# Kernel optimization log

Measured on AMD Instinct MI355X. Metric: run time of the kernel, lower is better.

## Reference

```python
import jax, jax.numpy as jnp
import numpy as np

N_JOBS, N_MACH = 30, 20
N = N_JOBS * N_MACH          # 600 nodes
IN_DIM = 2
H = 128                      # hidden_dim_feature_extractor
HA = 256                     # hidden_dim_actor
HC = 256                     # hidden_dim_critic
E = 9600                     # edges
BN_EPS = 1e-5


def setup_inputs() -> dict:
    key = jax.random.key(0)
    ks = jax.random.split(key, 16)
    init = lambda k, shp: (jax.random.normal(k, shp, jnp.float32) * 0.05)
    d = {
        "features": jax.random.normal(ks[0], (N, IN_DIM), jnp.float32),
        "edge_index": jax.random.randint(ks[1], (2, E), 0, N, jnp.int32),
        # GIN layer 0 MLP: Linear(IN,H) -> BN -> ReLU -> Linear(H,H)
        "g0_W0": init(ks[2], (IN_DIM, H)), "g0_b0": jnp.zeros((H,), jnp.float32),
        "g0_gamma": jnp.ones((H,), jnp.float32), "g0_beta": jnp.zeros((H,), jnp.float32),
        "g0_W1": init(ks[3], (H, H)), "g0_b1": jnp.zeros((H,), jnp.float32),
        # GIN layer 1 MLP: Linear(H,H) -> BN -> ReLU -> Linear(H,H)
        "g1_W0": init(ks[4], (H, H)), "g1_b0": jnp.zeros((H,), jnp.float32),
        "g1_gamma": jnp.ones((H,), jnp.float32), "g1_beta": jnp.zeros((H,), jnp.float32),
        "g1_W1": init(ks[5], (H, H)), "g1_b1": jnp.zeros((H,), jnp.float32),
        # actor MLP: Linear(3H,HA) -> ReLU -> Linear(HA,1)
        "a_W0": init(ks[6], (3 * H, HA)), "a_b0": jnp.zeros((HA,), jnp.float32),
        "a_W1": init(ks[7], (HA, 1)), "a_b1": jnp.zeros((1,), jnp.float32),
        # critic MLP: Linear(H,HC) -> ReLU -> Linear(HC,1)
        "c_W0": init(ks[8], (H, HC)), "c_b0": jnp.zeros((HC,), jnp.float32),
        "c_W1": init(ks[9], (HC, 1)), "c_b1": jnp.zeros((1,), jnp.float32),
    }
    return d


def _gin_mlp(h, W0, b0, gamma, beta, W1, b1):
    # Linear -> BatchNorm(train-mode batch stats) -> ReLU -> Linear
    h1 = h @ W0 + b0
    mu = h1.mean(axis=0)
    var = h1.var(axis=0)
    h1 = gamma * (h1 - mu) * jax.lax.rsqrt(var + BN_EPS) + beta
    return jax.nn.relu(h1) @ W1 + b1


def reference(features, edge_index,
              g0_W0, g0_b0, g0_gamma, g0_beta, g0_W1, g0_b1,
              g1_W0, g1_b0, g1_gamma, g1_beta, g1_W1, g1_b1,
              a_W0, a_b0, a_W1, a_b1,
              c_W0, c_b0, c_W1, c_b1):
    src, dst = edge_index[0], edge_index[1]

    def gin(x, *mlp_params):
        # GINConv with eps=0: MLP(x + sum_{j in N(i)} x_j)
        agg = jax.ops.segment_sum(x[src], dst, num_segments=N)
        return _gin_mlp(x + agg, *mlp_params)

    h = gin(features, g0_W0, g0_b0, g0_gamma, g0_beta, g0_W1, g0_b1)
    h = gin(h, g1_W0, g1_b0, g1_gamma, g1_beta, g1_W1, g1_b1)   # (N, H)

    # graph pooling: (ones/N) @ h  == mean over nodes
    ge = h.mean(axis=0, keepdims=True)                           # (1, H)
    value = jax.nn.relu(ge @ c_W0 + c_b0) @ c_W1 + c_b1          # (1, 1)

    # s_a_pairs row k (k = i*N + j): [ge, h[j] (tile), h[i] (repeat_interleave)]
    # Fuse concat + first actor matmul by splitting a_W0 into three H-blocks.
    Ws, Wn1, Wn2 = a_W0[:H], a_W0[H:2 * H], a_W0[2 * H:]
    pre = (ge @ Ws + a_b0)[None, :, :] + (h @ Wn1)[None, :, :] + (h @ Wn2)[:, None, :]
    logits = jax.nn.relu(pre).reshape(N * N, HA) @ a_W1 + a_b1   # (N^2, 1)
    pi = jax.nn.softmax(logits, axis=0)
    return pi, value
```

## Files before the change

### kernel.cpp

```cpp
#include <hip/hip_runtime.h>
#include <math.h>

#define N_NODES 600
#define N_EDGES 9600
#define HDIM    128
#define HA      256
#define HC      256
#define NN      360000
#define BN_EPS  1e-5f
#define NTILE   361

#define OFF_U      0
#define OFF_BCONST 1200
#define OFF_BF     1456
#define OFF_SUMZ   1584
#define OFF_SUMZ2  1712
#define OFF_R1SUM  1840
#define OFF_RACC   1968
#define OFF_MAXA   2224
#define OFF_SUMA   2736
#define OFF_CSR    3248
#define OFF_WF     13456
#define OFF_WC1    29840
#define OFF_WC2    62608
#define OFF_WGS    95376
#define OFF_Z      128144
#define OFF_A      204944
#define OFF_B      358544

typedef _Float16 h2 __attribute__((ext_vector_type(2)));
typedef _Float16 h4 __attribute__((ext_vector_type(4)));
typedef _Float16 h8 __attribute__((ext_vector_type(8)));

__device__ __forceinline__ float dot2acc(h2 a, h2 b, float c) {
#if __has_builtin(__builtin_amdgcn_fdot2)
  return __builtin_amdgcn_fdot2(a, b, c, false);
#else
  return c + (float)a.x * (float)b.x + (float)a.y * (float)b.y;
#endif
}

__device__ __forceinline__ h2 relu2(h2 x) {
  h2 z = {(_Float16)0, (_Float16)0};
#if __has_builtin(__builtin_elementwise_max)
  return __builtin_elementwise_max(x, z);
#else
  h2 r;
  r.x = x.x > z.x ? x.x : z.x;
  r.y = x.y > z.y ? x.y : z.y;
  return r;
#endif
}

__device__ __forceinline__ h4 toh4(float4 v) {
  h4 r;
  r.x = (_Float16)v.x; r.y = (_Float16)v.y;
  r.z = (_Float16)v.z; r.w = (_Float16)v.w;
  return r;
}

struct KP {
  const float* feat; const int* ei;
  const float *g0W0, *g0ga, *g0be, *g0W1, *g0b1;
  const float *g1W0, *g1ga, *g1be, *g1W1, *g1b1;
  const float *aW0, *ab0, *aW1;
  const float *cW0, *cb0, *cW1, *cb1;
  float* ws; float* out;
};

__global__ __launch_bounds__(256) void k_indep(KP p) {
  __shared__ float sm[1536];
  const int b = blockIdx.x, t = threadIdx.x;

  if (b < 25) {
    float* us = sm;
    if (t < 48) us[t] = 0.f;
    __syncthreads();
    const int lo = b * 24, hi = lo + 24;
    for (int e = t; e < N_EDGES; e += 256) {
      int d = p.ei[N_EDGES + e];
      if (d >= lo && d < hi) {
        int s = p.ei[e];
        atomicAdd(&us[2 * (d - lo)],     p.feat[2 * s]);
        atomicAdd(&us[2 * (d - lo) + 1], p.feat[2 * s + 1]);
      }
    }
    __syncthreads();
    if (t < 48) p.ws[OFF_U + b * 48 + t] = us[t] + p.feat[b * 48 + t];
  } else if (b == 25) {
    int* si = (int*)sm;
    int* cnt = si; int* bs = si + 600; int* off = si + 856;
    int* rs_g = (int*)(p.ws + OFF_CSR);
    int* src_g = rs_g + 604;
    for (int i = t; i < 600; i += 256) cnt[i] = 0;
    __syncthreads();
    for (int e = t; e < N_EDGES; e += 256) atomicAdd(&cnt[p.ei[N_EDGES + e]], 1);
    __syncthreads();
    int lsum = 0;
    if (t < 200) lsum = cnt[3 * t] + cnt[3 * t + 1] + cnt[3 * t + 2];
    bs[t] = lsum; __syncthreads();
    for (int d = 1; d < 256; d <<= 1) {
      int v = (t >= d) ? bs[t - d] : 0;
      __syncthreads();
      bs[t] += v;
      __syncthreads();
    }
    if (t < 200) {
      int base = bs[t] - lsum;
      off[3 * t] = base;
      off[3 * t + 1] = base + cnt[3 * t];
      off[3 * t + 2] = base + cnt[3 * t] + cnt[3 * t + 1];
    }
    if (t == 0) off[600] = N_EDGES;
    __syncthreads();
    for (int i = t; i < 601; i += 256) rs_g[i] = off[i];
    for (int i = t; i < 600; i += 256) cnt[i] = off[i];
    __syncthreads();
    for (int e = t; e < N_EDGES; e += 256) {
      int d = p.ei[N_EDGES + e];
      int pos = atomicAdd(&cnt[d], 1);
      src_g[pos] = p.ei[e];
    }
  } else if (b < 122) {
    int o = (b - 26) * 1024 + t * 4;
    int mat = o >> 15, rem = o & 32767;
    int j = rem >> 8, k = rem & 255;
    int rowbase = (mat == 0) ? HDIM : (mat == 1 ? 2 * HDIM : 0);
    const float* aw = p.aW0 + rowbase * HA + k;
    float4 acc = make_float4(0, 0, 0, 0);
#pragma unroll 8
    for (int m = 0; m < HDIM; m++) {
      float w = p.g1W1[j * HDIM + m];
      const float4 v = *(const float4*)(aw + m * HA);
      acc.x += w * v.x; acc.y += w * v.y; acc.z += w * v.z; acc.w += w * v.w;
    }
    int dst = (mat == 0) ? OFF_WC1 : (mat == 1 ? OFF_WC2 : OFF_WGS);
    *(float4*)(p.ws + dst + j * HA + k) = acc;
  } else if (b < 138) {
    int o = (b - 122) * 1024 + t * 4;
    int j = o >> 7, c = o & 127;
    float4 acc = make_float4(0, 0, 0, 0);
#pragma unroll 8
    for (int m = 0; m < HDIM; m++) {
      float w = p.g0W1[j * HDIM + m];
      const float4 v = *(const float4*)(p.g1W0 + m * HDIM + c);
      acc.x += w * v.x; acc.y += w * v.y; acc.z += w * v.z; acc.w += w * v.w;
    }
    *(float4*)(p.ws + OFF_WF + j * HDIM + c) = acc;
  } else {
    float acc = 0.f;
#pragma unroll 8
    for (int m = 0; m < HDIM; m++) {
      float gb = p.g1b1[m];
      acc += gb * (p.aW0[m * HA + t] + p.aW0[(HDIM + m) * HA + t] +
                   p.aW0[(2 * HDIM + m) * HA + t]);
    }
    p.ws[OFF_BCONST + t] = p.ab0[t] + acc;
    p.ws[OFF_RACC + t] = 0.f;
    if (t < 128) {
      float a2 = 0.f;
#pragma unroll 8
      for (int m = 0; m < HDIM; m++) a2 += p.g0b1[m] * p.g1W0[m * HDIM + t];
      p.ws[OFF_BF + t] = a2;
      p.ws[OFF_SUMZ + t] = 0.f;
      p.ws[OFF_SUMZ2 + t] = 0.f;
      p.ws[OFF_R1SUM + t] = 0.f;
    }
  }
}

__global__ __launch_bounds__(256) void k_zagg(KP p) {
  __shared__ float2 u2[600];
  __shared__ float bn[384];
  __shared__ float r0agg[512];
  __shared__ float red[256];
  __shared__ float wred[24];
  const int b = blockIdx.x, t = threadIdx.x, n0 = b * 4;
  const float2* ug = (const float2*)(p.ws + OFF_U);
  for (int i = t; i < 600; i += 256) u2[i] = ug[i];
  __syncthreads();
  float s0 = 0, s1 = 0, s00 = 0, s11 = 0, s01 = 0;
  for (int n = t; n < N_NODES; n += 256) {
    float u0 = u2[n].x, u1 = u2[n].y;
    s0 += u0; s1 += u1; s00 += u0 * u0; s11 += u1 * u1; s01 += u0 * u1;
  }
#pragma unroll
  for (int off = 32; off > 0; off >>= 1) {
    s0  += __shfl_xor(s0, off);  s1  += __shfl_xor(s1, off);
    s00 += __shfl_xor(s00, off); s11 += __shfl_xor(s11, off);
    s01 += __shfl_xor(s01, off);
  }
  const int wv = t >> 6, ln = t & 63;
  if (ln == 0) {
    wred[wv * 5 + 0] = s0;  wred[wv * 5 + 1] = s1;  wred[wv * 5 + 2] = s00;
    wred[wv * 5 + 3] = s11; wred[wv * 5 + 4] = s01;
  }
  __syncthreads();
  if (t < HDIM) {
    float tot[5];
#pragma unroll
    for (int q = 0; q < 5; q++)
      tot[q] = wred[q] + wred[5 + q] + wred[10 + q] + wred[15 + q];
    float m0 = tot[0] / 600.f, m1 = tot[1] / 600.f;
    float v00 = tot[2] / 600.f - m0 * m0;
    float v11 = tot[3] / 600.f - m1 * m1;
    float v01 = tot[4] / 600.f - m0 * m1;
    float W00 = p.g0W0[t], W01 = p.g0W0[HDIM + t];
    float var = W00 * W00 * v00 + W01 * W01 * v11 + 2.f * W00 * W01 * v01;
    float sc = p.g0ga[t] * rsqrtf(var + BN_EPS);
    float mu = m0 * W00 + m1 * W01;
    bn[t] = sc * W00; bn[128 + t] = sc * W01; bn[256 + t] = p.g0be[t] - mu * sc;
  }
  __syncthreads();
  const int* rs = (const int*)(p.ws + OFF_CSR);
  const int* srcv = rs + 604;
#pragma unroll
  for (int pq = 0; pq < 2; pq++) {
    int idx = pq * 256 + t, n = idx >> 7, c = idx & 127, node = n0 + n;
    float b0c = bn[c], b1c = bn[128 + c], b2c = bn[256 + c];
    float2 uo = u2[node];
    float acc = fmaxf(uo.x * b0c + uo.y * b1c + b2c, 0.f);
    int e0 = rs[node], e1 = rs[node + 1];
    for (int e = e0; e < e1; e++) {
      float2 us = u2[srcv[e]];
      acc += fmaxf(us.x * b0c + us.y * b1c + b2c, 0.f);
    }
    r0agg[n * 128 + c] = acc;
  }
  __syncthreads();
  const float* Wf = p.ws + OFF_WF;
  const float* bf = p.ws + OFF_BF;
  float zs = 0.f, zs2 = 0.f;
#pragma unroll
  for (int pq = 0; pq < 2; pq++) {
    int idx = pq * 256 + t, n = idx >> 7, c = idx & 127, node = n0 + n;
    const float* row = r0agg + n * 128;
    int deg = rs[node + 1] - rs[node];
    float acc = (1.f + (float)deg) * bf[c];
#pragma unroll 8
    for (int j = 0; j < HDIM; j++) acc += row[j] * Wf[j * HDIM + c];
    p.ws[OFF_Z + node * HDIM + c] = acc;
    zs += acc; zs2 += acc * acc;
  }
  red[t] = zs; __syncthreads();
  if (t < 128) atomicAdd(&p.ws[OFF_SUMZ + t], red[t] + red[t + 128]);
  __syncthreads();
  red[t] = zs2; __syncthreads();
  if (t < 128) atomicAdd(&p.ws[OFF_SUMZ2 + t], red[t] + red[t + 128]);
}

__global__ __launch_bounds__(256) void k_rab(KP p) {
  __shared__ float r1[4 * 128];
  __shared__ float scl[128], shf[128], rsum4[128];
  const int b = blockIdx.x, t = threadIdx.x, n0 = b * 4;
  if (t < 128) {
    float mu = p.ws[OFF_SUMZ + t] * (1.f / 600.f);
    float var = p.ws[OFF_SUMZ2 + t] * (1.f / 600.f) - mu * mu;
    float sc = p.g1ga[t] * rsqrtf(var + BN_EPS);
    scl[t] = sc; shf[t] = p.g1be[t] - mu * sc;
  }
  __syncthreads();
#pragma unroll
  for (int pq = 0; pq < 2; pq++) {
    int idx = pq * 256 + t, n = idx >> 7, j = idx & 127;
    float z = p.ws[OFF_Z + (n0 + n) * HDIM + j];
    r1[n * 128 + j] = fmaxf(z * scl[j] + shf[j], 0.f);
  }
  __syncthreads();
  if (t < 128) {
    float s = r1[t] + r1[128 + t] + r1[256 + t] + r1[384 + t];
    rsum4[t] = s;
    atomicAdd(&p.ws[OFF_R1SUM + t], s);
  }
  __syncthreads();
  const float* wc1 = p.ws + OFF_WC1;
  const float* wc2 = p.ws + OFF_WC2;
  const float* wgs = p.ws + OFF_WGS;
  float a0 = 0, a1 = 0, a2 = 0, a3 = 0, b0 = 0, b1 = 0, b2 = 0, b3 = 0, rc = 0;
#pragma unroll 4
  for (int j = 0; j < HDIM; j++) {
    float w1 = wc1[j * HA + t], w2 = wc2[j * HA + t], wg = wgs[j * HA + t];
    float r0v = r1[j], r1v = r1[128 + j], r2v = r1[256 + j], r3v = r1[384 + j];
    a0 += r0v * w1; a1 += r1v * w1; a2 += r2v * w1; a3 += r3v * w1;
    b0 += r0v * w2; b1 += r1v * w2; b2 += r2v * w2; b3 += r3v * w2;
    rc += rsum4[j] * wg;
  }
  atomicAdd(&p.ws[OFF_RACC + t], rc);
  float* A = p.ws + OFF_A; float* Bm = p.ws + OFF_B;
  A[n0 * HA + t] = a0; A[(n0 + 1) * HA + t] = a1;
  A[(n0 + 2) * HA + t] = a2; A[(n0 + 3) * HA + t] = a3;
  Bm[n0 * HA + t] = b0; Bm[(n0 + 1) * HA + t] = b1;
  Bm[(n0 + 2) * HA + t] = b2; Bm[(n0 + 3) * HA + t] = b3;
}

__global__ __launch_bounds__(256) void k_heads(KP p) {
  __shared__ h4 AsL[2048];
  __shared__ h4 BsL[2048];
  __shared__ h4 wlp[64];
  __shared__ h4 hsp[64];
  __shared__ float hsl[256];
  __shared__ float ge[128];
  __shared__ float geh[128];
  __shared__ float red[256];
  const int b = blockIdx.x, t = threadIdx.x;

  hsl[t] = p.ws[OFF_RACC + t] * (1.f / 600.f) + p.ws[OFF_BCONST + t];

  if (b == 0) {
    if (t < 128) ge[t] = p.ws[OFF_R1SUM + t] * (1.f / 600.f);
    __syncthreads();
    if (t < 128) {
      float a0 = p.g1b1[t], a1 = 0.f, a2 = 0.f, a3 = 0.f;
#pragma unroll 4
      for (int j = 0; j < HDIM; j += 4) {
        a0 += ge[j]     * p.g1W1[(j)     * HDIM + t];
        a1 += ge[j + 1] * p.g1W1[(j + 1) * HDIM + t];
        a2 += ge[j + 2] * p.g1W1[(j + 2) * HDIM + t];
        a3 += ge[j + 3] * p.g1W1[(j + 3) * HDIM + t];
      }
      geh[t] = (a0 + a1) + (a2 + a3);
    }
    __syncthreads();
    {
      float v0 = p.cb0[t], v1 = 0.f, v2 = 0.f, v3 = 0.f;
#pragma unroll 4
      for (int c = 0; c < HDIM; c += 4) {
        v0 += geh[c]     * p.cW0[(c)     * HC + t];
        v1 += geh[c + 1] * p.cW0[(c + 1) * HC + t];
        v2 += geh[c + 2] * p.cW0[(c + 2) * HC + t];
        v3 += geh[c + 3] * p.cW0[(c + 3) * HC + t];
      }
      float v = fmaxf((v0 + v1) + (v2 + v3), 0.f);
      red[t] = v * p.cW1[t];
    }
    __syncthreads();
    for (int off = 128; off > 0; off >>= 1) {
      if (t < off) red[t] += red[t + off];
      __syncthreads();
    }
    if (t == 0) p.out[NN] = red[0] + p.cb1[0];
  }
  __syncthreads();
  if (t < 64) {
    wlp[t] = toh4(*(const float4*)(p.aW1 + 4 * t));
    hsp[t] = toh4(*(const float4*)(hsl + 4 * t));
  }
  __syncthreads();

  const int tj = b % 19, ti = b / 19;
  const int j0 = tj * 32, i0 = ti * 32;
  const float* A  = p.ws + OFF_A;
  const float* Bm = p.ws + OFF_B;
#pragma unroll
  for (int q = 0; q < 8; q++) {
    int f = q * 256 + t;
    int r = f >> 6;
    int c4 = f & 63;
    int k = c4 * 4;
    int sw = c4 * 32 + (r ^ (c4 & 30));
    float4 av = (j0 + r < N_NODES) ? *(const float4*)(A + (j0 + r) * HA + k)
                                   : make_float4(0, 0, 0, 0);
    AsL[sw] = toh4(av) + hsp[c4];
    float4 bv = (i0 + r < N_NODES) ? *(const float4*)(Bm + (i0 + r) * HA + k)
                                   : make_float4(0, 0, 0, 0);
    BsL[sw] = toh4(bv);
  }
  __syncthreads();

  const int tx = t & 15, ty = t >> 4;
  const int jl = tx * 2, il = ty * 2;
  float a00 = 0, a01 = 0, a10 = 0, a11 = 0;
#pragma unroll 8
  for (int kk2 = 0; kk2 < 64; kk2++) {
    int s = kk2 & 30;
    h8 va = *(h8*)&AsL[kk2 * 32 + (jl ^ s)];
    h8 vb = *(h8*)&BsL[kk2 * 32 + (il ^ s)];
    h4 vw = wlp[kk2];
    h2 wlo = __builtin_shufflevector(vw, vw, 0, 1);
    h2 whi = __builtin_shufflevector(vw, vw, 2, 3);
    h2 aj0lo = __builtin_shufflevector(va, va, 0, 1);
    h2 aj0hi = __builtin_shufflevector(va, va, 2, 3);
    h2 aj1lo = __builtin_shufflevector(va, va, 4, 5);
    h2 aj1hi = __builtin_shufflevector(va, va, 6, 7);
    h2 bi0lo = __builtin_shufflevector(vb, vb, 0, 1);
    h2 bi0hi = __builtin_shufflevector(vb, vb, 2, 3);
    h2 bi1lo = __builtin_shufflevector(vb, vb, 4, 5);
    h2 bi1hi = __builtin_shufflevector(vb, vb, 6, 7);
    a00 = dot2acc(relu2(aj0lo + bi0lo), wlo, a00);
    a00 = dot2acc(relu2(aj0hi + bi0hi), whi, a00);
    a01 = dot2acc(relu2(aj1lo + bi0lo), wlo, a01);
    a01 = dot2acc(relu2(aj1hi + bi0hi), whi, a01);
    a10 = dot2acc(relu2(aj0lo + bi1lo), wlo, a10);
    a10 = dot2acc(relu2(aj0hi + bi1hi), whi, a10);
    a11 = dot2acc(relu2(aj1lo + bi1lo), wlo, a11);
    a11 = dot2acc(relu2(aj1hi + bi1hi), whi, a11);
  }

  const int gi = i0 + il, gj = j0 + jl;
  const bool vi0 = gi < N_NODES, vi1 = gi + 1 < N_NODES;
  const bool vj0 = gj < N_NODES, vj1 = gj + 1 < N_NODES;
  float m = -INFINITY;
  if (vi0 && vj0) m = fmaxf(m, a00);
  if (vi0 && vj1) m = fmaxf(m, a01);
  if (vi1 && vj0) m = fmaxf(m, a10);
  if (vi1 && vj1) m = fmaxf(m, a11);
  __syncthreads();
  red[t] = m;
  __syncthreads();
  for (int off = 128; off > 0; off >>= 1) {
    if (t < off) red[t] = fmaxf(red[t], red[t + off]);
    __syncthreads();
  }
  const float mb = red[0];
  float s = 0.f;
  if (vi0 && vj0) { float e = expf(a00 - mb); p.out[gi * N_NODES + gj] = e; s += e; }
  if (vi0 && vj1) { float e = expf(a01 - mb); p.out[gi * N_NODES + gj + 1] = e; s += e; }
  if (vi1 && vj0) { float e = expf(a10 - mb); p.out[(gi + 1) * N_NODES + gj] = e; s += e; }
  if (vi1 && vj1) { float e = expf(a11 - mb); p.out[(gi + 1) * N_NODES + gj + 1] = e; s += e; }
  __syncthreads();
  red[t] = s;
  __syncthreads();
  for (int off = 128; off > 0; off >>= 1) {
    if (t < off) red[t] += red[t + off];
    __syncthreads();
  }
  if (t == 0) { p.ws[OFF_MAXA + b] = mb; p.ws[OFF_SUMA + b] = red[0]; }
}

__global__ __launch_bounds__(256) void k_fin(KP p) {
  __shared__ float red[256];
  __shared__ float sc19[19];
  const int b = blockIdx.x, t = threadIdx.x;
  const float* maxa = p.ws + OFF_MAXA;
  const float* suma = p.ws + OFF_SUMA;
  float m = -INFINITY;
  if (t < NTILE) m = maxa[t];
  if (t + 256 < NTILE) m = fmaxf(m, maxa[t + 256]);
  red[t] = m;
  __syncthreads();
  for (int off = 128; off > 0; off >>= 1) {
    if (t < off) red[t] = fmaxf(red[t], red[t + off]);
    __syncthreads();
  }
  const float gmax = red[0];
  __syncthreads();
  float s = 0.f;
  if (t < NTILE) s += suma[t] * expf(maxa[t] - gmax);
  if (t + 256 < NTILE) s += suma[t + 256] * expf(maxa[t + 256] - gmax);
  red[t] = s;
  __syncthreads();
  for (int off = 128; off > 0; off >>= 1) {
    if (t < off) red[t] += red[t + off];
    __syncthreads();
  }
  const float invtot = 1.0f / red[0];
  const int ti = (b * 4) >> 5;
  if (t < 19) sc19[t] = expf(maxa[ti * 19 + t] - gmax) * invtot;
  __syncthreads();
#pragma unroll
  for (int pass = 0; pass < 3; pass++) {
    int f4 = pass * 256 + t;
    if (f4 < 600) {
      int r = f4 / 150, c4 = (f4 % 150) * 4;
      float* pp = p.out + (b * 4 + r) * N_NODES + c4;
      float4 v = *(const float4*)pp;
      float sc = sc19[c4 >> 5];
      v.x *= sc; v.y *= sc; v.z *= sc; v.w *= sc;
      *(float4*)pp = v;
    }
  }
}

extern "C" void kernel_launch(void* const* d_in, const int* in_sizes, int n_in,
                              void* d_out, int out_size, void* d_ws, size_t ws_size,
                              hipStream_t stream) {
  KP p;
  p.feat = (const float*)d_in[0];
  p.ei   = (const int*)  d_in[1];
  p.g0W0 = (const float*)d_in[2];
  p.g0ga = (const float*)d_in[4];  p.g0be = (const float*)d_in[5];
  p.g0W1 = (const float*)d_in[6];  p.g0b1 = (const float*)d_in[7];
  p.g1W0 = (const float*)d_in[8];
  p.g1ga = (const float*)d_in[10]; p.g1be = (const float*)d_in[11];
  p.g1W1 = (const float*)d_in[12]; p.g1b1 = (const float*)d_in[13];
  p.aW0  = (const float*)d_in[14]; p.ab0  = (const float*)d_in[15];
  p.aW1  = (const float*)d_in[16];
  p.cW0  = (const float*)d_in[18]; p.cb0  = (const float*)d_in[19];
  p.cW1  = (const float*)d_in[20]; p.cb1  = (const float*)d_in[21];
  p.ws   = (float*)d_ws;
  p.out  = (float*)d_out;

  k_indep<<<139,   256, 0, stream>>>(p);
  k_zagg <<<150,   256, 0, stream>>>(p);
  k_rab  <<<150,   256, 0, stream>>>(p);
  k_heads<<<NTILE, 256, 0, stream>>>(p);
  k_fin  <<<150,   256, 0, stream>>>(p);
}
```

Measured before the change: 79.75 us.

## Drop max-subtraction from softmax and move actor weight precompute into zagg

The softmax no longer computes per-tile maxima. Each tile writes exp(logit) directly and only block sums are reduced, so k_fin becomes a plain sum and scale. This removes two block reductions and the expf rescaling, at the risk of overflow if logits grow large. Separately, the actor-weight folding (WC1/WC2/WGS) and the bias-constant blocks move from k_indep into extra blocks of k_zagg, overlapping that work with the aggregation stage and shrinking the first kernel.

```diff
diff --git a/kernel.cpp b/kernel.cpp
--- a/kernel.cpp
+++ b/kernel.cpp
@@ -17,7 +17,6 @@
 #define OFF_SUMZ2  1712
 #define OFF_R1SUM  1840
 #define OFF_RACC   1968
-#define OFF_MAXA   2224
 #define OFF_SUMA   2736
 #define OFF_CSR    3248
 #define OFF_WF     13456
@@ -121,23 +120,8 @@
       int pos = atomicAdd(&cnt[d], 1);
       src_g[pos] = p.ei[e];
     }
-  } else if (b < 122) {
+  } else if (b < 42) {
     int o = (b - 26) * 1024 + t * 4;
-    int mat = o >> 15, rem = o & 32767;
-    int j = rem >> 8, k = rem & 255;
-    int rowbase = (mat == 0) ? HDIM : (mat == 1 ? 2 * HDIM : 0);
-    const float* aw = p.aW0 + rowbase * HA + k;
-    float4 acc = make_float4(0, 0, 0, 0);
-#pragma unroll 8
-    for (int m = 0; m < HDIM; m++) {
-      float w = p.g1W1[j * HDIM + m];
-      const float4 v = *(const float4*)(aw + m * HA);
-      acc.x += w * v.x; acc.y += w * v.y; acc.z += w * v.z; acc.w += w * v.w;
-    }
-    int dst = (mat == 0) ? OFF_WC1 : (mat == 1 ? OFF_WC2 : OFF_WGS);
-    *(float4*)(p.ws + dst + j * HA + k) = acc;
-  } else if (b < 138) {
-    int o = (b - 122) * 1024 + t * 4;
     int j = o >> 7, c = o & 127;
     float4 acc = make_float4(0, 0, 0, 0);
 #pragma unroll 8
@@ -148,14 +132,6 @@
     }
     *(float4*)(p.ws + OFF_WF + j * HDIM + c) = acc;
   } else {
-    float acc = 0.f;
-#pragma unroll 8
-    for (int m = 0; m < HDIM; m++) {
-      float gb = p.g1b1[m];
-      acc += gb * (p.aW0[m * HA + t] + p.aW0[(HDIM + m) * HA + t] +
-                   p.aW0[(2 * HDIM + m) * HA + t]);
-    }
-    p.ws[OFF_BCONST + t] = p.ab0[t] + acc;
     p.ws[OFF_RACC + t] = 0.f;
     if (t < 128) {
       float a2 = 0.f;
@@ -175,7 +151,38 @@
   __shared__ float r0agg[512];
   __shared__ float red[256];
   __shared__ float wred[24];
-  const int b = blockIdx.x, t = threadIdx.x, n0 = b * 4;
+  const int b = blockIdx.x, t = threadIdx.x;
+
+  if (b >= 150) {
+    if (b < 246) {
+      int o = (b - 150) * 1024 + t * 4;
+      int mat = o >> 15, rem = o & 32767;
+      int j = rem >> 8, k = rem & 255;
+      int rowbase = (mat == 0) ? HDIM : (mat == 1 ? 2 * HDIM : 0);
+      const float* aw = p.aW0 + rowbase * HA + k;
+      float4 acc = make_float4(0, 0, 0, 0);
+#pragma unroll 8
+      for (int m = 0; m < HDIM; m++) {
+        float w = p.g1W1[j * HDIM + m];
+        const float4 v = *(const float4*)(aw + m * HA);
+        acc.x += w * v.x; acc.y += w * v.y; acc.z += w * v.z; acc.w += w * v.w;
+      }
+      int dst = (mat == 0) ? OFF_WC1 : (mat == 1 ? OFF_WC2 : OFF_WGS);
+      *(float4*)(p.ws + dst + j * HA + k) = acc;
+    } else {
+      float acc = 0.f;
+#pragma unroll 8
+      for (int m = 0; m < HDIM; m++) {
+        float gb = p.g1b1[m];
+        acc += gb * (p.aW0[m * HA + t] + p.aW0[(HDIM + m) * HA + t] +
+                     p.aW0[(2 * HDIM + m) * HA + t]);
+      }
+      p.ws[OFF_BCONST + t] = p.ab0[t] + acc;
+    }
+    return;
+  }
+
+  const int n0 = b * 4;
   const float2* ug = (const float2*)(p.ws + OFF_U);
   for (int i = t; i < 600; i += 256) u2[i] = ug[i];
   __syncthreads();
@@ -399,24 +406,11 @@
   const int gi = i0 + il, gj = j0 + jl;
   const bool vi0 = gi < N_NODES, vi1 = gi + 1 < N_NODES;
   const bool vj0 = gj < N_NODES, vj1 = gj + 1 < N_NODES;
-  float m = -INFINITY;
-  if (vi0 && vj0) m = fmaxf(m, a00);
-  if (vi0 && vj1) m = fmaxf(m, a01);
-  if (vi1 && vj0) m = fmaxf(m, a10);
-  if (vi1 && vj1) m = fmaxf(m, a11);
-  __syncthreads();
-  red[t] = m;
-  __syncthreads();
-  for (int off = 128; off > 0; off >>= 1) {
-    if (t < off) red[t] = fmaxf(red[t], red[t + off]);
-    __syncthreads();
-  }
-  const float mb = red[0];
   float s = 0.f;
-  if (vi0 && vj0) { float e = expf(a00 - mb); p.out[gi * N_NODES + gj] = e; s += e; }
-  if (vi0 && vj1) { float e = expf(a01 - mb); p.out[gi * N_NODES + gj + 1] = e; s += e; }
-  if (vi1 && vj0) { float e = expf(a10 - mb); p.out[(gi + 1) * N_NODES + gj] = e; s += e; }
-  if (vi1 && vj1) { float e = expf(a11 - mb); p.out[(gi + 1) * N_NODES + gj + 1] = e; s += e; }
+  if (vi0 && vj0) { float e = __expf(a00); p.out[gi * N_NODES + gj] = e; s += e; }
+  if (vi0 && vj1) { float e = __expf(a01); p.out[gi * N_NODES + gj + 1] = e; s += e; }
+  if (vi1 && vj0) { float e = __expf(a10); p.out[(gi + 1) * N_NODES + gj] = e; s += e; }
+  if (vi1 && vj1) { float e = __expf(a11); p.out[(gi + 1) * N_NODES + gj + 1] = e; s += e; }
   __syncthreads();
   red[t] = s;
   __syncthreads();
@@ -424,39 +418,21 @@
     if (t < off) red[t] += red[t + off];
     __syncthreads();
   }
-  if (t == 0) { p.ws[OFF_MAXA + b] = mb; p.ws[OFF_SUMA + b] = red[0]; }
+  if (t == 0) p.ws[OFF_SUMA + b] = red[0];
 }
 
 __global__ __launch_bounds__(256) void k_fin(KP p) {
   __shared__ float red[256];
-  __shared__ float sc19[19];
   const int b = blockIdx.x, t = threadIdx.x;
-  const float* maxa = p.ws + OFF_MAXA;
   const float* suma = p.ws + OFF_SUMA;
-  float m = -INFINITY;
-  if (t < NTILE) m = maxa[t];
-  if (t + 256 < NTILE) m = fmaxf(m, maxa[t + 256]);
-  red[t] = m;
-  __syncthreads();
-  for (int off = 128; off > 0; off >>= 1) {
-    if (t < off) red[t] = fmaxf(red[t], red[t + off]);
-    __syncthreads();
-  }
-  const float gmax = red[0];
-  __syncthreads();
-  float s = 0.f;
-  if (t < NTILE) s += suma[t] * expf(maxa[t] - gmax);
-  if (t + 256 < NTILE) s += suma[t + 256] * expf(maxa[t + 256] - gmax);
+  float s = (t < NTILE ? suma[t] : 0.f) + (t + 256 < NTILE ? suma[t + 256] : 0.f);
   red[t] = s;
   __syncthreads();
   for (int off = 128; off > 0; off >>= 1) {
     if (t < off) red[t] += red[t + off];
     __syncthreads();
   }
-  const float invtot = 1.0f / red[0];
-  const int ti = (b * 4) >> 5;
-  if (t < 19) sc19[t] = expf(maxa[ti * 19 + t] - gmax) * invtot;
-  __syncthreads();
+  const float inv = 1.0f / red[0];
 #pragma unroll
   for (int pass = 0; pass < 3; pass++) {
     int f4 = pass * 256 + t;
@@ -464,8 +440,7 @@
       int r = f4 / 150, c4 = (f4 % 150) * 4;
       float* pp = p.out + (b * 4 + r) * N_NODES + c4;
       float4 v = *(const float4*)pp;
-      float sc = sc19[c4 >> 5];
-      v.x *= sc; v.y *= sc; v.z *= sc; v.w *= sc;
+      v.x *= inv; v.y *= inv; v.z *= inv; v.w *= inv;
       *(float4*)pp = v;
     }
   }
@@ -490,8 +465,8 @@
   p.ws   = (float*)d_ws;
   p.out  = (float*)d_out;
 
-  k_indep<<<139,   256, 0, stream>>>(p);
-  k_zagg <<<150,   256, 0, stream>>>(p);
+  k_indep<<<43,    256, 0, stream>>>(p);
+  k_zagg <<<247,   256, 0, stream>>>(p);
   k_rab  <<<150,   256, 0, stream>>>(p);
   k_heads<<<NTILE, 256, 0, stream>>>(p);
   k_fin  <<<150,   256, 0, stream>>>(p);
```

After: 78.41 us (median of 2 runs). No clear change (-1.7%).
